# Performance work log

Measured on AMD Instinct MI355X. Metric: run time of the kernel, lower is better.

## Reference

```python
import jax, jax.numpy as jnp
import numpy as np

B, L, D, H, DH, DEPTH, VOCAB = 8, 512, 256, 8, 64, 16, 5
INNER = 4 * D  # GLU feedforward inner dim = 1024
EPS = 1e-5

def _ln(x, g, b):
    mu = jnp.mean(x, -1, keepdims=True)
    var = jnp.mean(jnp.square(x - mu), -1, keepdims=True)
    return (x - mu) * jax.lax.rsqrt(var + EPS) * g + b

def setup_inputs() -> dict:
    key = jax.random.key(0)
    ks = jax.random.split(key, 24)
    s = 0.02
    seq = jax.random.randint(ks[0], (B, L), 0, VOCAB)
    lengths = jax.random.randint(ks[1], (B,), L // 2, L + 1)
    mask = jnp.arange(L)[None, :] < lengths[:, None]  # [B, L] bool padding mask
    f32 = jnp.float32
    return {
        "seq": seq,
        "mask": mask,
        "emb": jax.random.normal(ks[2], (VOCAB, D), f32) * s,
        "png": jnp.ones((D,), f32), "pnb": jnp.zeros((D,), f32),
        "ln1g": jnp.ones((DEPTH, D), f32), "ln1b": jnp.zeros((DEPTH, D), f32),
        "Wq": jax.random.normal(ks[3], (DEPTH, D, H * DH), f32) * s,
        "Wk": jax.random.normal(ks[4], (DEPTH, D, H * DH), f32) * s,
        "Wv": jax.random.normal(ks[5], (DEPTH, D, H * DH), f32) * s,
        "Wo": jax.random.normal(ks[6], (DEPTH, H * DH, D), f32) * s,
        "ln2g": jnp.ones((DEPTH, D), f32), "ln2b": jnp.zeros((DEPTH, D), f32),
        "W1": jax.random.normal(ks[7], (DEPTH, D, 2 * INNER), f32) * s,
        "b1": jnp.zeros((DEPTH, 2 * INNER), f32),
        "W2": jax.random.normal(ks[8], (DEPTH, INNER, D), f32) * s,
        "b2": jnp.zeros((DEPTH, D), f32),
        "fng": jnp.ones((D,), f32), "fnb": jnp.zeros((D,), f32),
        "Wout": jax.random.normal(ks[9], (D, 2), f32) * s,
        "bout": jnp.zeros((2,), f32),
    }

def _alibi_bias(n):
    # heads=8 is a power of two: slopes = 2^{-1}..2^{-8}
    slopes = 2.0 ** (-(jnp.arange(1, H + 1, dtype=jnp.float32)) * (8.0 / H))
    pos = jnp.arange(n, dtype=jnp.float32)
    rel = -jnp.abs(pos[None, :] - pos[:, None])  # [n, n]
    return slopes[:, None, None] * rel  # [H, n, n]

def _forward(seq, mask, emb, png, pnb, ln1g, ln1b, Wq, Wk, Wv, Wo,
             ln2g, ln2b, W1, b1, W2, b2, fng, fnb, Wout, bout):
    x = emb[seq]                      # [B, L, D]
    x = _ln(x, png, pnb)              # post_emb_norm
    bias = _alibi_bias(L)             # [H, L, L]
    kv_mask = mask[:, None, None, :]  # [B, 1, 1, L]
    scale = DH ** -0.5

    def layer(x, p):
        (g1, c1, wq, wk, wv, wo, g2, c2, w1, bb1, w2, bb2) = p
        h = _ln(x, g1, c1)
        q = (h @ wq).reshape(B, L, H, DH).transpose(0, 2, 1, 3)  # bhld
        k = (h @ wk).reshape(B, L, H, DH).transpose(0, 2, 1, 3)
        v = (h @ wv).reshape(B, L, H, DH).transpose(0, 2, 1, 3)
        scores = jnp.einsum('bhid,bhjd->bhij', q, k) * scale + bias
        scores = jnp.where(kv_mask, scores, jnp.float32(-1e9))
        a = jax.nn.softmax(scores, axis=-1)
        o = jnp.einsum('bhij,bhjd->bhid', a, v)
        o = o.transpose(0, 2, 1, 3).reshape(B, L, H * DH) @ wo
        x = x + o
        h2 = _ln(x, g2, c2)
        u = h2 @ w1 + bb1
        val, gate = jnp.split(u, 2, axis=-1)  # GLU: x * gelu(gate)
        x = x + (val * jax.nn.gelu(gate, approximate=False)) @ w2 + bb2
        return x, None

    x, _ = jax.lax.scan(layer, x, (ln1g, ln1b, Wq, Wk, Wv, Wo, ln2g, ln2b, W1, b1, W2, b2))
    x = _ln(x, fng, fnb)              # final encoder norm
    return x @ Wout + bout            # [B, L, 2]

def reference(seq, mask, emb, png, pnb, ln1g, ln1b, Wq, Wk, Wv, Wo,
              ln2g, ln2b, W1, b1, W2, b2, fng, fnb, Wout, bout):
    return _forward(seq, mask, emb, png, pnb, ln1g, ln1b, Wq, Wk, Wv, Wo,
                    ln2g, ln2b, W1, b1, W2, b2, fng, fnb, Wout, bout)
```

## Files before the change

### kernel.cpp

```cpp
#include <hip/hip_runtime.h>
#include <cstdint>
#include <cstddef>

#define BB 8
#define LL 512
#define DD 256
#define HH 8
#define DHD 64
#define NLAYER 16
#define HDH 512
#define IN2 2048
#define IN1 1024

typedef __attribute__((ext_vector_type(8))) short short8;
typedef __attribute__((ext_vector_type(4))) float floatx4;
typedef __attribute__((ext_vector_type(4))) unsigned short ushort4v;
typedef unsigned short u16;

__device__ __forceinline__ floatx4 mfma16(short8 a, short8 b, floatx4 c) {
  return __builtin_amdgcn_mfma_f32_16x16x32_bf16(a, b, c, 0, 0, 0);
}

__device__ __forceinline__ u16 f2b(float f) {
  union { float f; unsigned u; } x; x.f = f;
  unsigned u = x.u + 0x7fffu + ((x.u >> 16) & 1u);
  return (u16)(u >> 16);
}
__device__ __forceinline__ float b2f(u16 s) {
  union { unsigned u; float f; } x; x.u = ((unsigned)s) << 16;
  return x.f;
}

__device__ __forceinline__ float wave_sum(float s) {
#pragma unroll
  for (int off = 32; off; off >>= 1) s += __shfl_xor(s, off);
  return s;
}

__device__ __forceinline__ void gload_lds16(const u16* g, u16* l) {
  __builtin_amdgcn_global_load_lds((__attribute__((address_space(1))) void*)g,
                                   (__attribute__((address_space(3))) void*)l,
                                   16, 0, 0);
}

template <int NSLOTS, int NTHREADS = 256>
__device__ __forceinline__ void stage_tile(const u16* __restrict__ g, int rowstride,
                                           u16* lds, int tid) {
  int wave = tid >> 6, lane = tid & 63;
#pragma unroll
  for (int j = 0; j < NSLOTS / NTHREADS; ++j) {
    int sbase = j * NTHREADS + wave * 64;
    int slot = sbase + lane;
    int row = slot >> 3;
    int kg = (slot & 7) ^ (row & 7);
    gload_lds16(g + (size_t)row * rowstride + kg * 8, lds + sbase * 8);
  }
}

__device__ __forceinline__ short8 ld_frag(const u16* T, int row, int kg) {
  return *(const short8*)&T[(row << 6) + (((kg ^ row) & 7) << 3)];
}

__device__ __forceinline__ short8 ld_frag128(const u16* T, int row, int kg) {
  int pg = (kg & 8) | ((kg ^ row) & 7);
  return *(const short8*)&T[(row << 7) + (pg << 3)];
}

__device__ __forceinline__ float4 ln_math(const float* __restrict__ x,
                                          const float* __restrict__ g,
                                          const float* __restrict__ b, int t) {
  float4 v = *(const float4*)(x + t * 4);
  float s = wave_sum(v.x + v.y + v.z + v.w);
  float mu = s * (1.0f / DD);
  float dx = v.x - mu, dy = v.y - mu, dz = v.z - mu, dw = v.w - mu;
  float ss = wave_sum(dx * dx + dy * dy + dz * dz + dw * dw);
  float r = rsqrtf(ss * (1.0f / DD) + 1e-5f);
  float4 gg = *(const float4*)(g + t * 4);
  float4 bb = *(const float4*)(b + t * 4);
  float4 o;
  o.x = dx * r * gg.x + bb.x;
  o.y = dy * r * gg.y + bb.y;
  o.z = dz * r * gg.z + bb.z;
  o.w = dw * r * gg.w + bb.w;
  return o;
}

__global__ __launch_bounds__(256) void embed_ln_kernel(
    const int* __restrict__ seq, const float* __restrict__ emb,
    const float* __restrict__ png, const float* __restrict__ pnb,
    const float* __restrict__ g1, const float* __restrict__ b1,
    float* __restrict__ X, u16* __restrict__ H) {
  int row = blockIdx.x * 4 + (threadIdx.x >> 6), t = threadIdx.x & 63;
  int tok = seq[row];
  float4 o = ln_math(emb + (size_t)tok * DD, png, pnb, t);
  *(float4*)(X + (size_t)row * DD + t * 4) = o;
  float s = wave_sum(o.x + o.y + o.z + o.w);
  float mu = s * (1.0f / DD);
  float dx = o.x - mu, dy = o.y - mu, dz = o.z - mu, dw = o.w - mu;
  float ss = wave_sum(dx * dx + dy * dy + dz * dz + dw * dw);
  float r = rsqrtf(ss * (1.0f / DD) + 1e-5f);
  float4 gg = *(const float4*)(g1 + t * 4);
  float4 bb = *(const float4*)(b1 + t * 4);
  ushort4v o4;
  o4[0] = f2b(dx * r * gg.x + bb.x);
  o4[1] = f2b(dy * r * gg.y + bb.y);
  o4[2] = f2b(dz * r * gg.z + bb.z);
  o4[3] = f2b(dw * r * gg.w + bb.w);
  *(ushort4v*)(H + (size_t)row * DD + t * 4) = o4;
}

#define WBUF_LAYER 1310720
__global__ __launch_bounds__(256) void prep_weights_kernel(
    const float* __restrict__ Wq, const float* __restrict__ Wk,
    const float* __restrict__ Wv, const float* __restrict__ Wo,
    const float* __restrict__ W1, const float* __restrict__ W2,
    u16* __restrict__ wbuf_all) {
  __shared__ float tile[32][33];
  int l = blockIdx.x / 1280;
  int bx = blockIdx.x % 1280;
  int tid = threadIdx.x;
  const float* wq = Wq + (size_t)l * DD * HDH;
  const float* wk = Wk + (size_t)l * DD * HDH;
  const float* wv = Wv + (size_t)l * DD * HDH;
  const float* wo = Wo + (size_t)l * HDH * DD;
  const float* w1 = W1 + (size_t)l * DD * IN2;
  const float* w2 = W2 + (size_t)l * IN1 * DD;
  u16* wbuf = wbuf_all + (size_t)l * WBUF_LAYER;

  const float* src; int srcld; u16* dst; int dstld; int dn0, k0, scol0;
  int packW1 = 0;
  if (bx < 384) {
    int t = bx; dn0 = (t % 48) * 32; k0 = (t / 48) * 32;
    scol0 = dn0 & 511;
    src = (dn0 < 512) ? wq : ((dn0 < 1024) ? wk : wv);
    srcld = 512; dst = wbuf; dstld = 256;
  } else if (bx < 512) {
    int t = bx - 384; dn0 = (t % 8) * 32; k0 = (t / 8) * 32; scol0 = dn0;
    src = wo; srcld = 256; dst = wbuf + 393216; dstld = 512;
  } else if (bx < 1024) {
    int t = bx - 512; dn0 = (t % 64) * 32; k0 = (t / 64) * 32; scol0 = dn0;
    src = w1; srcld = 2048; dst = wbuf + 524288; dstld = 256; packW1 = 1;
  } else {
    int t = bx - 1024; dn0 = (t % 8) * 32; k0 = (t / 8) * 32; scol0 = dn0;
    src = w2; srcld = 256; dst = wbuf + 1048576; dstld = 1024;
  }
  int r = tid >> 3, c4 = (tid & 7) * 4;
  float4 v = *(const float4*)&src[(size_t)(k0 + r) * srcld + scol0 + c4];
  tile[r][c4 + 0] = v.x; tile[r][c4 + 1] = v.y;
  tile[r][c4 + 2] = v.z; tile[r][c4 + 3] = v.w;
  __syncthreads();
  int n = tid >> 3, kk = (tid & 7) * 4;
  int drow = dn0 + n;
  if (packW1) {
    if (drow < 1024) drow = ((drow >> 4) << 5) | (drow & 15);
    else { int nn = drow - 1024; drow = (((nn >> 4) << 5) + 16) | (nn & 15); }
  }
  ushort4v o4;
  o4[0] = f2b(tile[kk + 0][n]); o4[1] = f2b(tile[kk + 1][n]);
  o4[2] = f2b(tile[kk + 2][n]); o4[3] = f2b(tile[kk + 3][n]);
  *(ushort4v*)&dst[(size_t)drow * dstld + k0 + kk] = o4;
}

__global__ __launch_bounds__(256) void gemm_qkv(
    const u16* __restrict__ A, const u16* __restrict__ BT,
    u16* __restrict__ qk, u16* __restrict__ vT) {
  __shared__ __align__(16) u16 As[2][128 * 64];
  __shared__ __align__(16) u16 Bs[2][96 * 64];
  int tid = threadIdx.x;
  int wave = tid >> 6, lane = tid & 63;
  int lm = lane & 15, quad = lane >> 4;
  int wr = wave >> 1, wc = wave & 1;
  int n0 = blockIdx.x * 96, m0 = blockIdx.y * 128;
  const u16* Ab = A + (size_t)m0 * DD;
  const u16* Bb = BT + (size_t)n0 * DD;

  floatx4 acc[4][3];
#pragma unroll
  for (int mf = 0; mf < 4; ++mf)
#pragma unroll
    for (int nf = 0; nf < 3; ++nf)
#pragma unroll
      for (int r = 0; r < 4; ++r) acc[mf][nf][r] = 0.0f;

  stage_tile<1024>(Ab, DD, As[0], tid);
  stage_tile<768>(Bb, DD, Bs[0], tid);
  __syncthreads();
#pragma unroll
  for (int it = 0; it < 4; ++it) {
    if (it < 3) {
      stage_tile<1024>(Ab + (it + 1) * 64, DD, As[(it + 1) & 1], tid);
      stage_tile<768>(Bb + (it + 1) * 64, DD, Bs[(it + 1) & 1], tid);
    }
    const u16* Ac = As[it & 1];
    const u16* Bc = Bs[it & 1];
#pragma unroll
    for (int kc = 0; kc < 2; ++kc) {
      short8 af[4], bf[3];
#pragma unroll
      for (int mf = 0; mf < 4; ++mf)
        af[mf] = ld_frag(Ac, wr * 64 + mf * 16 + lm, kc * 4 + quad);
#pragma unroll
      for (int nf = 0; nf < 3; ++nf)
        bf[nf] = ld_frag(Bc, wc * 48 + nf * 16 + lm, kc * 4 + quad);
#pragma unroll
      for (int mf = 0; mf < 4; ++mf)
#pragma unroll
        for (int nf = 0; nf < 3; ++nf)
          acc[mf][nf] = mfma16(af[mf], bf[nf], acc[mf][nf]);
    }
    if (it < 3) __syncthreads();
  }
#pragma unroll
  for (int mf = 0; mf < 4; ++mf)
#pragma unroll
    for (int nf = 0; nf < 3; ++nf) {
      int colf = n0 + wc * 48 + nf * 16;
      if (colf < 1024) {
#pragma unroll
        for (int r = 0; r < 4; ++r) {
          int row = m0 + wr * 64 + mf * 16 + quad * 4 + r;
          qk[(size_t)row * 1024 + colf + lm] = f2b(acc[mf][nf][r]);
        }
      } else {
        int token0 = m0 + wr * 64 + mf * 16 + quad * 4;
        int hd = colf + lm - 1024;
        int b = token0 >> 9, key = token0 & 511;
        ushort4v p4;
#pragma unroll
        for (int r = 0; r < 4; ++r) p4[r] = f2b(acc[mf][nf][r]);
        *(ushort4v*)&vT[((size_t)(b * 8 + (hd >> 6)) * 64 + (hd & 63)) * 512 + key] = p4;
      }
    }
}

__global__ __launch_bounds__(256) void gemm_ffn1(
    const u16* __restrict__ A, const u16* __restrict__ BTp,
    const float* __restrict__ b1, u16* __restrict__ G) {
  __shared__ __align__(16) u16 As[2][128 * 64];
  __shared__ __align__(16) u16 Bs[2][128 * 64];
  int tid = threadIdx.x;
  int wave = tid >> 6, lane = tid & 63;
  int lm = lane & 15, quad = lane >> 4;
  int wr = wave >> 1, wc = wave & 1;
  int n0 = blockIdx.x * 128, m0 = blockIdx.y * 128;
  const u16* Ab = A + (size_t)m0 * DD;
  const u16* Bb = BTp + (size_t)n0 * DD;

  floatx4 acc[4][4];
#pragma unroll
  for (int mf = 0; mf < 4; ++mf)
#pragma unroll
    for (int nf = 0; nf < 4; ++nf)
#pragma unroll
      for (int r = 0; r < 4; ++r) acc[mf][nf][r] = 0.0f;

  stage_tile<1024>(Ab, DD, As[0], tid);
  stage_tile<1024>(Bb, DD, Bs[0], tid);
  __syncthreads();
#pragma unroll
  for (int it = 0; it < 4; ++it) {
    if (it < 3) {
      stage_tile<1024>(Ab + (it + 1) * 64, DD, As[(it + 1) & 1], tid);
      stage_tile<1024>(Bb + (it + 1) * 64, DD, Bs[(it + 1) & 1], tid);
    }
    const u16* Ac = As[it & 1];
    const u16* Bc = Bs[it & 1];
#pragma unroll
    for (int kc = 0; kc < 2; ++kc) {
      short8 af[4], bf[4];
#pragma unroll
      for (int mf = 0; mf < 4; ++mf)
        af[mf] = ld_frag(Ac, wr * 64 + mf * 16 + lm, kc * 4 + quad);
#pragma unroll
      for (int nf = 0; nf < 4; ++nf)
        bf[nf] = ld_frag(Bc, wc * 64 + nf * 16 + lm, kc * 4 + quad);
#pragma unroll
      for (int mf = 0; mf < 4; ++mf)
#pragma unroll
        for (int nf = 0; nf < 4; ++nf)
          acc[mf][nf] = mfma16(af[mf], bf[nf], acc[mf][nf]);
    }
    if (it < 3) __syncthreads();
  }
  int p0 = (n0 + wc * 64) >> 5;
#pragma unroll
  for (int j = 0; j < 2; ++j) {
    int gcol = (p0 + j) * 16 + lm;
    float bv = b1[gcol], bg = b1[1024 + gcol];
#pragma unroll
    for (int mf = 0; mf < 4; ++mf)
#pragma unroll
      for (int r = 0; r < 4; ++r) {
        int row = m0 + wr * 64 + mf * 16 + quad * 4 + r;
        float val = acc[mf][2 * j][r] + bv;
        float gate = acc[mf][2 * j + 1][r] + bg;
        float ge = 0.5f * gate * (1.0f + erff(gate * 0.70710678118654752440f));
        G[(size_t)row * IN1 + gcol] = f2b(val * ge);
      }
  }
}

__global__ __launch_bounds__(512) void gemm_row_ln(
    const u16* __restrict__ A, int lda, const u16* __restrict__ BT, int K,
    const float* __restrict__ bias, float* __restrict__ X,
    const float* __restrict__ lng, const float* __restrict__ lnb,
    u16* __restrict__ Hout,
    const float* __restrict__ Wout, const float* __restrict__ bout,
    float* __restrict__ outp) {
  __shared__ __align__(16) u16 As[2][16 * 128];
  __shared__ __align__(16) u16 Bs[2][256 * 128];
  int tid = threadIdx.x;
  int wave = tid >> 6, lane = tid & 63;
  int lm = lane & 15, quad = lane >> 4;
  int m0 = blockIdx.x * 16;

  floatx4 acc[2];
#pragma unroll
  for (int nf = 0; nf < 2; ++nf)
#pragma unroll
    for (int r = 0; r < 4; ++r) acc[nf][r] = 0.0f;

  const u16* Ab = A + (size_t)m0 * lda;

  auto stageA = [&](int k0, u16* dst) {
    if (wave < 4) {
      int sbase = wave * 64;
      int slot = sbase + lane;
      int row = slot >> 4, pg = slot & 15;
      int kg = (pg & 8) | ((pg ^ row) & 7);
      gload_lds16(Ab + (size_t)row * lda + k0 + kg * 8, dst + sbase * 8);
    }
  };
  auto stageB = [&](int k0, u16* dst) {
#pragma unroll
    for (int j = 0; j < 8; ++j) {
      int sbase = j * 512 + wave * 64;
      int slot = sbase + lane;
      int row = slot >> 4, pg = slot & 15;
      int kg = (pg & 8) | ((pg ^ row) & 7);
      gload_lds16(BT + (size_t)row * K + k0 + kg * 8, dst + sbase * 8);
    }
  };

  stageA(0, As[0]);
  stageB(0, Bs[0]);
  __syncthreads();
  int iters = K >> 7;
  for (int it = 0; it < iters; ++it) {
    if (it + 1 < iters) {
      stageA((it + 1) * 128, As[(it + 1) & 1]);
      stageB((it + 1) * 128, Bs[(it + 1) & 1]);
    }
    const u16* Ac = As[it & 1];
    const u16* Bc = Bs[it & 1];
#pragma unroll
    for (int kc = 0; kc < 4; ++kc) {
      short8 af = ld_frag128(Ac, lm, kc * 4 + quad);
#pragma unroll
      for (int nf = 0; nf < 2; ++nf) {
        short8 bf = ld_frag128(Bc, wave * 32 + nf * 16 + lm, kc * 4 + quad);
        acc[nf] = mfma16(af, bf, acc[nf]);
      }
    }
    if (it + 1 < iters) __syncthreads();
  }
  __syncthreads();
  float* xs = (float*)Bs[0];
#pragma unroll
  for (int nf = 0; nf < 2; ++nf) {
    int col = wave * 32 + nf * 16 + lm;
    float bv = bias ? bias[col] : 0.0f;
#pragma unroll
    for (int r = 0; r < 4; ++r) {
      int row = quad * 4 + r;
      float v = acc[nf][r] + bv + X[(size_t)(m0 + row) * DD + col];
      X[(size_t)(m0 + row) * DD + col] = v;
      xs[row * DD + col] = v;
    }
  }
  __syncthreads();
  float4 gg = *(const float4*)(lng + lane * 4);
  float4 bb = *(const float4*)(lnb + lane * 4);
#pragma unroll
  for (int rr = 0; rr < 2; ++rr) {
    int row = wave * 2 + rr;
    float4 v = *(const float4*)&xs[row * DD + lane * 4];
    float s = wave_sum(v.x + v.y + v.z + v.w);
    float mu = s * (1.0f / DD);
    float dx = v.x - mu, dy = v.y - mu, dz = v.z - mu, dw = v.w - mu;
    float ss = wave_sum(dx * dx + dy * dy + dz * dz + dw * dw);
    float rc = rsqrtf(ss * (1.0f / DD) + 1e-5f);
    float o0 = dx * rc * gg.x + bb.x;
    float o1 = dy * rc * gg.y + bb.y;
    float o2 = dz * rc * gg.z + bb.z;
    float o3 = dw * rc * gg.w + bb.w;
    ushort4v o4;
    o4[0] = f2b(o0); o4[1] = f2b(o1); o4[2] = f2b(o2); o4[3] = f2b(o3);
    *(ushort4v*)(Hout + (size_t)(m0 + row) * DD + lane * 4) = o4;
    if (Wout) {
      int d0 = lane * 4;
      float s0 = o0 * Wout[d0 * 2] + o1 * Wout[(d0 + 1) * 2] +
                 o2 * Wout[(d0 + 2) * 2] + o3 * Wout[(d0 + 3) * 2];
      float s1 = o0 * Wout[d0 * 2 + 1] + o1 * Wout[(d0 + 1) * 2 + 1] +
                 o2 * Wout[(d0 + 2) * 2 + 1] + o3 * Wout[(d0 + 3) * 2 + 1];
      s0 = wave_sum(s0);
      s1 = wave_sum(s1);
      if (lane == 0) {
        outp[(size_t)(m0 + row) * 2 + 0] = s0 + bout[0];
        outp[(size_t)(m0 + row) * 2 + 1] = s1 + bout[1];
      }
    }
  }
}

__global__ __launch_bounds__(512) void attn_mfma_kernel(
    const u16* __restrict__ qk, const u16* __restrict__ vT,
    const int* __restrict__ mask_raw, u16* __restrict__ O) {
  __shared__ __align__(16) u16 Ks[2][64 * 64];
  __shared__ __align__(16) u16 Vs[2][64 * 64];
  __shared__ __align__(16) u16 Ps[8][16][72];
  __shared__ __align__(16) float madd[64];

  const int tid = threadIdx.x, wave = tid >> 6, lane = tid & 63;
  const int lm = lane & 15, quad = lane >> 4;
  const int qb = blockIdx.x, h = blockIdx.y, b = blockIdx.z;
  const float slope = exp2f(-(float)(h + 1));

  int w0 = mask_raw[0];
  int mmode = (w0 == 1) ? 0 : ((w0 == 0x3f800000) ? 2 : 1);
  const int krow_base = b * LL;

  int ntv = 8;
#pragma unroll
  for (int t = 7; t >= 0; --t) {
    bool tv;
    int gi = krow_base + t * 64;
    if (mmode == 0) tv = mask_raw[gi] != 0;
    else if (mmode == 1) tv = ((const signed char*)mask_raw)[gi] != 0;
    else tv = ((const float*)mask_raw)[gi] != 0.0f;
    if (!tv) ntv = t;
  }

  const int q0 = qb * 128 + wave * 16;
  const int qg = b * LL + q0;
  const float qpos = (float)(q0 + lm);

  const u16* qp = qk + (size_t)(qg + lm) * 1024 + h * 64 + quad * 8;
  short8 qf0 = *(const short8*)qp;
  short8 qf1 = *(const short8*)(qp + 32);

  floatx4 oc[4];
#pragma unroll
  for (int nf = 0; nf < 4; ++nf)
#pragma unroll
    for (int r = 0; r < 4; ++r) oc[nf][r] = 0.0f;
  float mrow = -1e30f, lrow = 0.0f;

  const u16* kbase_p = qk + (size_t)krow_base * 1024 + 512 + h * 64;
  const u16* vbase = vT + (size_t)(b * 8 + h) * 64 * 512;

  stage_tile<512, 512>(kbase_p, 1024, Ks[0], tid);
  stage_tile<512, 512>(vbase, 512, Vs[0], tid);
  if (tid < 64) {
    int gi = krow_base + (ntv - 1) * 64 + tid;
    bool valid;
    if (mmode == 0) valid = mask_raw[gi] != 0;
    else if (mmode == 1) valid = ((const signed char*)mask_raw)[gi] != 0;
    else valid = ((const float*)mask_raw)[gi] != 0.0f;
    madd[tid] = valid ? 0.0f : -1e9f;
  }
  __syncthreads();

  for (int t = 0; t < ntv; ++t) {
    int k0 = t * 64;
    if (t + 1 < ntv) {
      stage_tile<512, 512>(kbase_p + (size_t)(t + 1) * 64 * 1024, 1024,
                           Ks[(t + 1) & 1], tid);
      stage_tile<512, 512>(vbase + (t + 1) * 64, 512, Vs[(t + 1) & 1], tid);
    }
    const u16* Kc = Ks[t & 1];
    const u16* Vc = Vs[t & 1];
    bool bnd = (t == ntv - 1);

    float sc[4][4];
    float tmax = -3e38f;
#pragma unroll
    for (int nt = 0; nt < 4; ++nt) {
      floatx4 pc;
#pragma unroll
      for (int r = 0; r < 4; ++r) pc[r] = 0.0f;
      short8 kf0 = ld_frag(Kc, nt * 16 + lm, quad);
      short8 kf1 = ld_frag(Kc, nt * 16 + lm, 4 + quad);
      pc = mfma16(kf0, qf0, pc);
      pc = mfma16(kf1, qf1, pc);
      float kbase = (float)(k0 + nt * 16 + quad * 4);
#pragma unroll
      for (int r = 0; r < 4; ++r) {
        float s = pc[r] * 0.125f - slope * fabsf(qpos - (kbase + r));
        sc[nt][r] = s;
      }
      if (bnd) {
        float4 ma = *(const float4*)&madd[nt * 16 + quad * 4];
#pragma unroll
        for (int r = 0; r < 4; ++r) sc[nt][r] += ((const float*)&ma)[r];
      }
#pragma unroll
      for (int r = 0; r < 4; ++r) tmax = fmaxf(tmax, sc[nt][r]);
    }
    tmax = fmaxf(tmax, __shfl_xor(tmax, 16));
    tmax = fmaxf(tmax, __shfl_xor(tmax, 32));
    float nm = fmaxf(mrow, tmax);
    float alpha = __expf(mrow - nm);
    mrow = nm;
    float rsum = 0.0f;
#pragma unroll
    for (int nt = 0; nt < 4; ++nt)
#pragma unroll
      for (int r = 0; r < 4; ++r) {
        float p = __expf(sc[nt][r] - nm);
        sc[nt][r] = p;
        rsum += p;
      }
    rsum += __shfl_xor(rsum, 16);
    rsum += __shfl_xor(rsum, 32);
    lrow = lrow * alpha + rsum;
    float av[4];
#pragma unroll
    for (int r = 0; r < 4; ++r) av[r] = __shfl(alpha, quad * 4 + r);
#pragma unroll
    for (int nf = 0; nf < 4; ++nf)
#pragma unroll
      for (int r = 0; r < 4; ++r) oc[nf][r] *= av[r];
#pragma unroll
    for (int nt = 0; nt < 4; ++nt) {
      ushort4v p4;
#pragma unroll
      for (int r = 0; r < 4; ++r) p4[r] = f2b(sc[nt][r]);
      *(ushort4v*)&Ps[wave][lm][nt * 16 + quad * 4] = p4;
    }
#pragma unroll
    for (int kc = 0; kc < 2; ++kc) {
      short8 af = *(const short8*)&Ps[wave][lm][kc * 32 + quad * 8];
#pragma unroll
      for (int nf = 0; nf < 4; ++nf) {
        short8 bv = ld_frag(Vc, nf * 16 + lm, kc * 4 + quad);
        oc[nf] = mfma16(af, bv, oc[nf]);
      }
    }
    if (t + 1 < ntv) __syncthreads();
  }
  float rl = 1.0f / lrow;
  float rv[4];
#pragma unroll
  for (int r = 0; r < 4; ++r) rv[r] = __shfl(rl, quad * 4 + r);
#pragma unroll
  for (int nf = 0; nf < 4; ++nf)
#pragma unroll
    for (int r = 0; r < 4; ++r) {
      int qq = qg + quad * 4 + r;
      O[(size_t)qq * HDH + h * 64 + nf * 16 + lm] = f2b(oc[nf][r] * rv[r]);
    }
}

extern "C" void kernel_launch(void* const* d_in, const int* in_sizes, int n_in,
                              void* d_out, int out_size, void* d_ws, size_t ws_size,
                              hipStream_t stream) {
  const int* seq = (const int*)d_in[0];
  const int* mask = (const int*)d_in[1];
  const float* emb = (const float*)d_in[2];
  const float* png = (const float*)d_in[3];
  const float* pnb = (const float*)d_in[4];
  const float* ln1g = (const float*)d_in[5];
  const float* ln1b = (const float*)d_in[6];
  const float* Wq = (const float*)d_in[7];
  const float* Wk = (const float*)d_in[8];
  const float* Wv = (const float*)d_in[9];
  const float* Wo = (const float*)d_in[10];
  const float* ln2g = (const float*)d_in[11];
  const float* ln2b = (const float*)d_in[12];
  const float* W1 = (const float*)d_in[13];
  const float* b1 = (const float*)d_in[14];
  const float* W2 = (const float*)d_in[15];
  const float* b2 = (const float*)d_in[16];
  const float* fng = (const float*)d_in[17];
  const float* fnb = (const float*)d_in[18];
  const float* Wout = (const float*)d_in[19];
  const float* bout = (const float*)d_in[20];
  float* out = (float*)d_out;

  uint8_t* wsb = (uint8_t*)d_ws;
  float* x = (float*)(wsb + 0);
  u16* hb = (u16*)(wsb + 4194304);
  u16* wbuf = (u16*)(wsb + 6291456);
  u16* qk = (u16*)(wsb + 48234496);
  u16* vT = (u16*)(wsb + 56623104);
  u16* obuf = (u16*)(wsb + 60817408);
  u16* gbuf = (u16*)(wsb + 65011712);

  const int M = BB * LL;

  prep_weights_kernel<<<16 * 1280, 256, 0, stream>>>(Wq, Wk, Wv, Wo, W1, W2, wbuf);
  embed_ln_kernel<<<M / 4, 256, 0, stream>>>(seq, emb, png, pnb, ln1g, ln1b, x, hb);

  for (int l = 0; l < NLAYER; ++l) {
    u16* wl = wbuf + (size_t)l * WBUF_LAYER;

    gemm_qkv<<<dim3(1536 / 96, M / 128), 256, 0, stream>>>(hb, wl, qk, vT);

    attn_mfma_kernel<<<dim3(LL / 128, HH, BB), 512, 0, stream>>>(qk, vT, mask, obuf);

    gemm_row_ln<<<M / 16, 512, 0, stream>>>(
        obuf, HDH, wl + 393216, HDH, nullptr, x,
        ln2g + l * DD, ln2b + l * DD, hb, nullptr, nullptr, nullptr);

    gemm_ffn1<<<dim3(IN2 / 128, M / 128), 256, 0, stream>>>(
        hb, wl + 524288, b1 + (size_t)l * IN2, gbuf);

    const float* ng = (l < NLAYER - 1) ? (ln1g + (l + 1) * DD) : fng;
    const float* nb = (l < NLAYER - 1) ? (ln1b + (l + 1) * DD) : fnb;
    const float* wo_p = (l == NLAYER - 1) ? Wout : nullptr;
    const float* bo_p = (l == NLAYER - 1) ? bout : nullptr;
    float* out_p = (l == NLAYER - 1) ? out : nullptr;
    gemm_row_ln<<<M / 16, 512, 0, stream>>>(
        gbuf, IN1, wl + 1048576, IN1, b2 + (size_t)l * DD, x, ng, nb, hb,
        wo_p, bo_p, out_p);
  }

  (void)in_sizes; (void)n_in; (void)out_size; (void)ws_size;
}
```

Baseline: 1.223 ms.

## Fuse QKV projection into attention kernel, recomputing K/V per query tile

```diff
diff --git a/kernel.cpp b/kernel.cpp
--- a/kernel.cpp
+++ b/kernel.cpp
@@ -64,6 +64,26 @@
 __device__ __forceinline__ short8 ld_frag128(const u16* T, int row, int kg) {
   int pg = (kg & 8) | ((kg ^ row) & 7);
   return *(const short8*)&T[(row << 7) + (pg << 3)];
+}
+
+template <int NSLOTS>
+__device__ __forceinline__ void stage_tile256(const u16* __restrict__ g,
+                                              int rowstride, u16* lds, int tid) {
+  int wave = tid >> 6, lane = tid & 63;
+#pragma unroll
+  for (int j = 0; j < NSLOTS / 512; ++j) {
+    int sbase = j * 512 + wave * 64;
+    int slot = sbase + lane;
+    int row = slot >> 5;
+    int g32 = slot & 31;
+    int kg = (g32 & 24) | ((g32 ^ row) & 7);
+    gload_lds16(g + (size_t)row * rowstride + kg * 8, lds + sbase * 8);
+  }
+}
+
+__device__ __forceinline__ short8 ld_frag256(const u16* T, int row, int g) {
+  int pg = (g & 24) | ((g ^ row) & 7);
+  return *(const short8*)&T[(row << 8) + (pg << 3)];
 }
 
 __device__ __forceinline__ float4 ln_math(const float* __restrict__ x,
@@ -161,75 +181,208 @@
   *(ushort4v*)&dst[(size_t)drow * dstld + k0 + kk] = o4;
 }
 
-__global__ __launch_bounds__(256) void gemm_qkv(
-    const u16* __restrict__ A, const u16* __restrict__ BT,
-    u16* __restrict__ qk, u16* __restrict__ vT) {
-  __shared__ __align__(16) u16 As[2][128 * 64];
-  __shared__ __align__(16) u16 Bs[2][96 * 64];
-  int tid = threadIdx.x;
-  int wave = tid >> 6, lane = tid & 63;
-  int lm = lane & 15, quad = lane >> 4;
-  int wr = wave >> 1, wc = wave & 1;
-  int n0 = blockIdx.x * 96, m0 = blockIdx.y * 128;
-  const u16* Ab = A + (size_t)m0 * DD;
-  const u16* Bb = BT + (size_t)n0 * DD;
-
-  floatx4 acc[4][3];
-#pragma unroll
-  for (int mf = 0; mf < 4; ++mf)
-#pragma unroll
-    for (int nf = 0; nf < 3; ++nf)
-#pragma unroll
-      for (int r = 0; r < 4; ++r) acc[mf][nf][r] = 0.0f;
-
-  stage_tile<1024>(Ab, DD, As[0], tid);
-  stage_tile<768>(Bb, DD, Bs[0], tid);
-  __syncthreads();
-#pragma unroll
-  for (int it = 0; it < 4; ++it) {
-    if (it < 3) {
-      stage_tile<1024>(Ab + (it + 1) * 64, DD, As[(it + 1) & 1], tid);
-      stage_tile<768>(Bb + (it + 1) * 64, DD, Bs[(it + 1) & 1], tid);
-    }
-    const u16* Ac = As[it & 1];
-    const u16* Bc = Bs[it & 1];
+__global__ __launch_bounds__(512, 2) void qkv_attn_kernel(
+    const u16* __restrict__ hb, const u16* __restrict__ wqkv,
+    const int* __restrict__ mask_raw, u16* __restrict__ O) {
+  __shared__ __align__(16) u16 smem[76928];
+  u16* Wb = smem;
+  u16* Ab = smem + 32768;
+  u16* Qs = smem + 49152;
+  u16* Ks = smem + 58368;
+  u16* Vs = smem + 62976;
+  u16* Ps = smem + 67584;
+  float* madd = (float*)(smem + 76800);
+
+  const int tid = threadIdx.x, wave = tid >> 6, lane = tid & 63;
+  const int lm = lane & 15, quad = lane >> 4;
+  const int qt = blockIdx.x, h = blockIdx.y, b = blockIdx.z;
+  const float slope = exp2f(-(float)(h + 1));
+
+  int w0 = mask_raw[0];
+  int mmode = (w0 == 1) ? 0 : ((w0 == 0x3f800000) ? 2 : 1);
+  const int krow_base = b * LL;
+
+  int ntv = 8;
+#pragma unroll
+  for (int t = 7; t >= 0; --t) {
+    bool tv;
+    int gi = krow_base + t * 64;
+    if (mmode == 0) tv = mask_raw[gi] != 0;
+    else if (mmode == 1) tv = ((const signed char*)mask_raw)[gi] != 0;
+    else tv = ((const float*)mask_raw)[gi] != 0.0f;
+    if (!tv) ntv = t;
+  }
+
+  stage_tile256<4096>(hb + (size_t)(b * LL + qt * 128) * DD, DD, Wb, tid);
+  stage_tile256<2048>(wqkv + (size_t)(h * 64) * DD, DD, Ab, tid);
+  __syncthreads();
+  {
+    floatx4 qacc[4];
+#pragma unroll
+    for (int nf = 0; nf < 4; ++nf)
+#pragma unroll
+      for (int r = 0; r < 4; ++r) qacc[nf][r] = 0.0f;
+#pragma unroll
+    for (int kc = 0; kc < 8; ++kc) {
+      short8 af = ld_frag256(Wb, wave * 16 + lm, kc * 4 + quad);
+#pragma unroll
+      for (int nf = 0; nf < 4; ++nf) {
+        short8 bf = ld_frag256(Ab, nf * 16 + lm, kc * 4 + quad);
+        qacc[nf] = mfma16(af, bf, qacc[nf]);
+      }
+    }
+#pragma unroll
+    for (int nf = 0; nf < 4; ++nf)
+#pragma unroll
+      for (int r = 0; r < 4; ++r)
+        Qs[(wave * 16 + quad * 4 + r) * 72 + nf * 16 + lm] = f2b(qacc[nf][r]);
+  }
+  short8 qf0 = *(const short8*)&Qs[(wave * 16 + lm) * 72 + quad * 8];
+  short8 qf1 = *(const short8*)&Qs[(wave * 16 + lm) * 72 + 32 + quad * 8];
+  __syncthreads();
+
+  stage_tile256<2048>(wqkv + (size_t)(512 + h * 64) * DD, DD, Wb, tid);
+  stage_tile256<2048>(wqkv + (size_t)(1024 + h * 64) * DD, DD, Wb + 16384, tid);
+  stage_tile256<2048>(hb + (size_t)(b * LL) * DD, DD, Ab, tid);
+  if (tid < 64) {
+    int gi = krow_base + (ntv - 1) * 64 + tid;
+    bool valid;
+    if (mmode == 0) valid = mask_raw[gi] != 0;
+    else if (mmode == 1) valid = ((const signed char*)mask_raw)[gi] != 0;
+    else valid = ((const float*)mask_raw)[gi] != 0.0f;
+    madd[tid] = valid ? 0.0f : -1e9f;
+  }
+  __syncthreads();
+
+  const int q0 = qt * 128 + wave * 16;
+  const int qg = b * LL + q0;
+  const float qpos = (float)(q0 + lm);
+
+  floatx4 oc[4];
+#pragma unroll
+  for (int nf = 0; nf < 4; ++nf)
+#pragma unroll
+    for (int r = 0; r < 4; ++r) oc[nf][r] = 0.0f;
+  float mrow = -1e30f, lrow = 0.0f;
+
+  for (int t = 0; t < ntv; ++t) {
+    int k0 = t * 64;
+    {
+      floatx4 kv[4];
+#pragma unroll
+      for (int nf = 0; nf < 4; ++nf)
+#pragma unroll
+        for (int r = 0; r < 4; ++r) kv[nf][r] = 0.0f;
+      int arow = (wave & 3) * 16 + lm;
+      int bbase = (wave < 4) ? 0 : 64;
+#pragma unroll
+      for (int kc = 0; kc < 8; ++kc) {
+        short8 af = ld_frag256(Ab, arow, kc * 4 + quad);
+#pragma unroll
+        for (int nf = 0; nf < 4; ++nf) {
+          short8 bf = ld_frag256(Wb, bbase + nf * 16 + lm, kc * 4 + quad);
+          kv[nf] = mfma16(af, bf, kv[nf]);
+        }
+      }
+      if (wave < 4) {
+#pragma unroll
+        for (int nf = 0; nf < 4; ++nf)
+#pragma unroll
+          for (int r = 0; r < 4; ++r)
+            Ks[((wave & 3) * 16 + quad * 4 + r) * 72 + nf * 16 + lm] =
+                f2b(kv[nf][r]);
+      } else {
+#pragma unroll
+        for (int nf = 0; nf < 4; ++nf) {
+          ushort4v p4;
+#pragma unroll
+          for (int r = 0; r < 4; ++r) p4[r] = f2b(kv[nf][r]);
+          *(ushort4v*)&Vs[(nf * 16 + lm) * 72 + (wave & 3) * 16 + quad * 4] = p4;
+        }
+      }
+    }
+    __syncthreads();
+    if (t + 1 < ntv)
+      stage_tile256<2048>(hb + (size_t)(b * LL + (t + 1) * 64) * DD, DD, Ab, tid);
+
+    bool bnd = (t == ntv - 1);
+    float sc[4][4];
+    float tmax = -3e38f;
+#pragma unroll
+    for (int nt = 0; nt < 4; ++nt) {
+      floatx4 pc;
+#pragma unroll
+      for (int r = 0; r < 4; ++r) pc[r] = 0.0f;
+      short8 kf0 = *(const short8*)&Ks[(nt * 16 + lm) * 72 + quad * 8];
+      short8 kf1 = *(const short8*)&Ks[(nt * 16 + lm) * 72 + 32 + quad * 8];
+      pc = mfma16(kf0, qf0, pc);
+      pc = mfma16(kf1, qf1, pc);
+      float kbase = (float)(k0 + nt * 16 + quad * 4);
+#pragma unroll
+      for (int r = 0; r < 4; ++r) {
+        float s = pc[r] * 0.125f - slope * fabsf(qpos - (kbase + r));
+        sc[nt][r] = s;
+      }
+      if (bnd) {
+        float4 ma = *(const float4*)&madd[nt * 16 + quad * 4];
+#pragma unroll
+        for (int r = 0; r < 4; ++r) sc[nt][r] += ((const float*)&ma)[r];
+      }
+#pragma unroll
+      for (int r = 0; r < 4; ++r) tmax = fmaxf(tmax, sc[nt][r]);
+    }
+    tmax = fmaxf(tmax, __shfl_xor(tmax, 16));
+    tmax = fmaxf(tmax, __shfl_xor(tmax, 32));
+    float nm = fmaxf(mrow, tmax);
+    float alpha = __expf(mrow - nm);
+    mrow = nm;
+    float rsum = 0.0f;
+#pragma unroll
+    for (int nt = 0; nt < 4; ++nt)
+#pragma unroll
+      for (int r = 0; r < 4; ++r) {
+        float p = __expf(sc[nt][r] - nm);
+        sc[nt][r] = p;
+        rsum += p;
+      }
+    rsum += __shfl_xor(rsum, 16);
+    rsum += __shfl_xor(rsum, 32);
+    lrow = lrow * alpha + rsum;
+    float av[4];
+#pragma unroll
+    for (int r = 0; r < 4; ++r) av[r] = __shfl(alpha, quad * 4 + r);
+#pragma unroll
+    for (int nf = 0; nf < 4; ++nf)
+#pragma unroll
+      for (int r = 0; r < 4; ++r) oc[nf][r] *= av[r];
+#pragma unroll
+    for (int nt = 0; nt < 4; ++nt) {
+      ushort4v p4;
+#pragma unroll
+      for (int r = 0; r < 4; ++r) p4[r] = f2b(sc[nt][r]);
+      *(ushort4v*)&Ps[(wave * 16 + lm) * 72 + nt * 16 + quad * 4] = p4;
+    }
 #pragma unroll
     for (int kc = 0; kc < 2; ++kc) {
-      short8 af[4], bf[3];
-#pragma unroll
-      for (int mf = 0; mf < 4; ++mf)
-        af[mf] = ld_frag(Ac, wr * 64 + mf * 16 + lm, kc * 4 + quad);
-#pragma unroll
-      for (int nf = 0; nf < 3; ++nf)
-        bf[nf] = ld_frag(Bc, wc * 48 + nf * 16 + lm, kc * 4 + quad);
-#pragma unroll
-      for (int mf = 0; mf < 4; ++mf)
-#pragma unroll
-        for (int nf = 0; nf < 3; ++nf)
-          acc[mf][nf] = mfma16(af[mf], bf[nf], acc[mf][nf]);
-    }
-    if (it < 3) __syncthreads();
-  }
-#pragma unroll
-  for (int mf = 0; mf < 4; ++mf)
-#pragma unroll
-    for (int nf = 0; nf < 3; ++nf) {
-      int colf = n0 + wc * 48 + nf * 16;
-      if (colf < 1024) {
-#pragma unroll
-        for (int r = 0; r < 4; ++r) {
-          int row = m0 + wr * 64 + mf * 16 + quad * 4 + r;
-          qk[(size_t)row * 1024 + colf + lm] = f2b(acc[mf][nf][r]);
-        }
-      } else {
-        int token0 = m0 + wr * 64 + mf * 16 + quad * 4;
-        int hd = colf + lm - 1024;
-        int b = token0 >> 9, key = token0 & 511;
-        ushort4v p4;
-#pragma unroll
-        for (int r = 0; r < 4; ++r) p4[r] = f2b(acc[mf][nf][r]);
-        *(ushort4v*)&vT[((size_t)(b * 8 + (hd >> 6)) * 64 + (hd & 63)) * 512 + key] = p4;
-      }
+      short8 af = *(const short8*)&Ps[(wave * 16 + lm) * 72 + kc * 32 + quad * 8];
+#pragma unroll
+      for (int nf = 0; nf < 4; ++nf) {
+        short8 bv = *(const short8*)&Vs[(nf * 16 + lm) * 72 + kc * 32 + quad * 8];
+        oc[nf] = mfma16(af, bv, oc[nf]);
+      }
+    }
+    __syncthreads();
+  }
+  float rl = 1.0f / lrow;
+  float rv[4];
+#pragma unroll
+  for (int r = 0; r < 4; ++r) rv[r] = __shfl(rl, quad * 4 + r);
+#pragma unroll
+  for (int nf = 0; nf < 4; ++nf)
+#pragma unroll
+    for (int r = 0; r < 4; ++r) {
+      int qq = qg + quad * 4 + r;
+      O[(size_t)qq * HDH + h * 64 + nf * 16 + lm] = f2b(oc[nf][r] * rv[r]);
     }
 }
 
@@ -413,155 +566,6 @@
   }
 }
 
-__global__ __launch_bounds__(512) void attn_mfma_kernel(
-    const u16* __restrict__ qk, const u16* __restrict__ vT,
-    const int* __restrict__ mask_raw, u16* __restrict__ O) {
-  __shared__ __align__(16) u16 Ks[2][64 * 64];
-  __shared__ __align__(16) u16 Vs[2][64 * 64];
-  __shared__ __align__(16) u16 Ps[8][16][72];
-  __shared__ __align__(16) float madd[64];
-
-  const int tid = threadIdx.x, wave = tid >> 6, lane = tid & 63;
-  const int lm = lane & 15, quad = lane >> 4;
-  const int qb = blockIdx.x, h = blockIdx.y, b = blockIdx.z;
-  const float slope = exp2f(-(float)(h + 1));
-
-  int w0 = mask_raw[0];
-  int mmode = (w0 == 1) ? 0 : ((w0 == 0x3f800000) ? 2 : 1);
-  const int krow_base = b * LL;
-
-  int ntv = 8;
-#pragma unroll
-  for (int t = 7; t >= 0; --t) {
-    bool tv;
-    int gi = krow_base + t * 64;
-    if (mmode == 0) tv = mask_raw[gi] != 0;
-    else if (mmode == 1) tv = ((const signed char*)mask_raw)[gi] != 0;
-    else tv = ((const float*)mask_raw)[gi] != 0.0f;
-    if (!tv) ntv = t;
-  }
-
-  const int q0 = qb * 128 + wave * 16;
-  const int qg = b * LL + q0;
-  const float qpos = (float)(q0 + lm);
-
-  const u16* qp = qk + (size_t)(qg + lm) * 1024 + h * 64 + quad * 8;
-  short8 qf0 = *(const short8*)qp;
-  short8 qf1 = *(const short8*)(qp + 32);
-
-  floatx4 oc[4];
-#pragma unroll
-  for (int nf = 0; nf < 4; ++nf)
-#pragma unroll
-    for (int r = 0; r < 4; ++r) oc[nf][r] = 0.0f;
-  float mrow = -1e30f, lrow = 0.0f;
-
-  const u16* kbase_p = qk + (size_t)krow_base * 1024 + 512 + h * 64;
-  const u16* vbase = vT + (size_t)(b * 8 + h) * 64 * 512;
-
-  stage_tile<512, 512>(kbase_p, 1024, Ks[0], tid);
-  stage_tile<512, 512>(vbase, 512, Vs[0], tid);
-  if (tid < 64) {
-    int gi = krow_base + (ntv - 1) * 64 + tid;
-    bool valid;
-    if (mmode == 0) valid = mask_raw[gi] != 0;
-    else if (mmode == 1) valid = ((const signed char*)mask_raw)[gi] != 0;
-    else valid = ((const float*)mask_raw)[gi] != 0.0f;
-    madd[tid] = valid ? 0.0f : -1e9f;
-  }
-  __syncthreads();
-
-  for (int t = 0; t < ntv; ++t) {
-    int k0 = t * 64;
-    if (t + 1 < ntv) {
-      stage_tile<512, 512>(kbase_p + (size_t)(t + 1) * 64 * 1024, 1024,
-                           Ks[(t + 1) & 1], tid);
-      stage_tile<512, 512>(vbase + (t + 1) * 64, 512, Vs[(t + 1) & 1], tid);
-    }
-    const u16* Kc = Ks[t & 1];
-    const u16* Vc = Vs[t & 1];
-    bool bnd = (t == ntv - 1);
-
-    float sc[4][4];
-    float tmax = -3e38f;
-#pragma unroll
-    for (int nt = 0; nt < 4; ++nt) {
-      floatx4 pc;
-#pragma unroll
-      for (int r = 0; r < 4; ++r) pc[r] = 0.0f;
-      short8 kf0 = ld_frag(Kc, nt * 16 + lm, quad);
-      short8 kf1 = ld_frag(Kc, nt * 16 + lm, 4 + quad);
-      pc = mfma16(kf0, qf0, pc);
-      pc = mfma16(kf1, qf1, pc);
-      float kbase = (float)(k0 + nt * 16 + quad * 4);
-#pragma unroll
-      for (int r = 0; r < 4; ++r) {
-        float s = pc[r] * 0.125f - slope * fabsf(qpos - (kbase + r));
-        sc[nt][r] = s;
-      }
-      if (bnd) {
-        float4 ma = *(const float4*)&madd[nt * 16 + quad * 4];
-#pragma unroll
-        for (int r = 0; r < 4; ++r) sc[nt][r] += ((const float*)&ma)[r];
-      }
-#pragma unroll
-      for (int r = 0; r < 4; ++r) tmax = fmaxf(tmax, sc[nt][r]);
-    }
-    tmax = fmaxf(tmax, __shfl_xor(tmax, 16));
-    tmax = fmaxf(tmax, __shfl_xor(tmax, 32));
-    float nm = fmaxf(mrow, tmax);
-    float alpha = __expf(mrow - nm);
-    mrow = nm;
-    float rsum = 0.0f;
-#pragma unroll
-    for (int nt = 0; nt < 4; ++nt)
-#pragma unroll
-      for (int r = 0; r < 4; ++r) {
-        float p = __expf(sc[nt][r] - nm);
-        sc[nt][r] = p;
-        rsum += p;
-      }
-    rsum += __shfl_xor(rsum, 16);
-    rsum += __shfl_xor(rsum, 32);
-    lrow = lrow * alpha + rsum;
-    float av[4];
-#pragma unroll
-    for (int r = 0; r < 4; ++r) av[r] = __shfl(alpha, quad * 4 + r);
-#pragma unroll
-    for (int nf = 0; nf < 4; ++nf)
-#pragma unroll
-      for (int r = 0; r < 4; ++r) oc[nf][r] *= av[r];
-#pragma unroll
-    for (int nt = 0; nt < 4; ++nt) {
-      ushort4v p4;
-#pragma unroll
-      for (int r = 0; r < 4; ++r) p4[r] = f2b(sc[nt][r]);
-      *(ushort4v*)&Ps[wave][lm][nt * 16 + quad * 4] = p4;
-    }
-#pragma unroll
-    for (int kc = 0; kc < 2; ++kc) {
-      short8 af = *(const short8*)&Ps[wave][lm][kc * 32 + quad * 8];
-#pragma unroll
-      for (int nf = 0; nf < 4; ++nf) {
-        short8 bv = ld_frag(Vc, nf * 16 + lm, kc * 4 + quad);
-        oc[nf] = mfma16(af, bv, oc[nf]);
-      }
-    }
-    if (t + 1 < ntv) __syncthreads();
-  }
-  float rl = 1.0f / lrow;
-  float rv[4];
-#pragma unroll
-  for (int r = 0; r < 4; ++r) rv[r] = __shfl(rl, quad * 4 + r);
-#pragma unroll
-  for (int nf = 0; nf < 4; ++nf)
-#pragma unroll
-    for (int r = 0; r < 4; ++r) {
-      int qq = qg + quad * 4 + r;
-      O[(size_t)qq * HDH + h * 64 + nf * 16 + lm] = f2b(oc[nf][r] * rv[r]);
-    }
-}
-
 extern "C" void kernel_launch(void* const* d_in, const int* in_sizes, int n_in,
                               void* d_out, int out_size, void* d_ws, size_t ws_size,
                               hipStream_t stream) {
@@ -592,10 +596,8 @@
   float* x = (float*)(wsb + 0);
   u16* hb = (u16*)(wsb + 4194304);
   u16* wbuf = (u16*)(wsb + 6291456);
-  u16* qk = (u16*)(wsb + 48234496);
-  u16* vT = (u16*)(wsb + 56623104);
-  u16* obuf = (u16*)(wsb + 60817408);
-  u16* gbuf = (u16*)(wsb + 65011712);
+  u16* obuf = (u16*)(wsb + 48234496);
+  u16* gbuf = (u16*)(wsb + 52428800);
 
   const int M = BB * LL;
 
@@ -605,9 +607,7 @@
   for (int l = 0; l < NLAYER; ++l) {
     u16* wl = wbuf + (size_t)l * WBUF_LAYER;
 
-    gemm_qkv<<<dim3(1536 / 96, M / 128), 256, 0, stream>>>(hb, wl, qk, vT);
-
-    attn_mfma_kernel<<<dim3(LL / 128, HH, BB), 512, 0, stream>>>(qk, vT, mask, obuf);
+    qkv_attn_kernel<<<dim3(4, HH, BB), 512, 0, stream>>>(hb, wl, mask, obuf);
 
     gemm_row_ln<<<M / 16, 512, 0, stream>>>(
         obuf, HDH, wl + 393216, HDH, nullptr, x,
```

Measured after the change: 1.252 ms. 1.02x slower.
